# Optimization experiments

Hardware: AMD Instinct MI355X
Metric: run time of the kernel (lower is better)

The kernel has to match this reference:

```python
import jax, jax.numpy as jnp
import numpy as np

EPS = 1e-5
HD = 16          # hidden_dim
OC = 256         # out_chs
NH = 8           # num_heads (groups of qkv conv)
DV = OC // (2 * HD)  # per-head value dim = 8


def conv_bn_silu(x, w, gamma, beta, mean, var, stride=1, pad=1, groups=1):
    # Conv2d(bias=False) + BatchNorm2d(eval) + SiLU, NCHW/OIHW
    y = jax.lax.conv_general_dilated(
        x, w, (stride, stride), [(pad, pad), (pad, pad)],
        dimension_numbers=('NCHW', 'OIHW', 'NCHW'),
        feature_group_count=groups)
    inv = gamma * jax.lax.rsqrt(var + EPS)
    y = y * inv[None, :, None, None] + (beta - mean * inv)[None, :, None, None]
    return y * jax.nn.sigmoid(y)


def _bn_params(key, c):
    k1, k2, k3, k4 = jax.random.split(key, 4)
    g = 1.0 + 0.1 * jax.random.normal(k1, (c,), jnp.float32)
    b = 0.1 * jax.random.normal(k2, (c,), jnp.float32)
    m = 0.1 * jax.random.normal(k3, (c,), jnp.float32)
    v = jax.random.uniform(k4, (c,), jnp.float32, 0.5, 1.5)
    return g, b, m, v


def setup_inputs() -> dict:
    key = jax.random.key(0)
    ks = jax.random.split(key, 8)
    B, C, H, W = 16, 256, 80, 80
    qkv_out = HD * 2 + OC // 2  # 160
    d = {}
    d['x'] = jax.random.normal(ks[0], (B, C, H, W), jnp.float32)
    # qkv_conv: grouped 3x3, groups=NH -> in per group = C//NH
    d['qkv_w'] = jax.random.normal(ks[1], (qkv_out, C // NH, 3, 3), jnp.float32) * 0.05
    d['qkv_g'], d['qkv_b'], d['qkv_m'], d['qkv_v'] = _bn_params(ks[2], qkv_out)
    # hidden_conv: dense 3x3
    d['hid_w'] = jax.random.normal(ks[3], (OC, C, 3, 3), jnp.float32) * 0.02
    d['hid_g'], d['hid_b'], d['hid_m'], d['hid_v'] = _bn_params(ks[4], OC)
    # out_conv: 1x1 on (OC//2*3) channels
    d['out_w'] = jax.random.normal(ks[5], (OC, OC // 2 * 3, 1, 1), jnp.float32) * 0.05
    d['out_g'], d['out_b'], d['out_m'], d['out_v'] = _bn_params(ks[6], OC)
    return d


def reference(x, qkv_w, qkv_g, qkv_b, qkv_m, qkv_v,
              hid_w, hid_g, hid_b, hid_m, hid_v,
              out_w, out_g, out_b, out_m, out_v):
    B, C, H, W = x.shape
    N = H * W
    qkv = conv_bn_silu(x, qkv_w, qkv_g, qkv_b, qkv_m, qkv_v, stride=1, pad=1, groups=NH)
    q = qkv[:, :HD]               # (B, HD, H, W)
    k = qkv[:, HD:2 * HD]
    v = qkv[:, 2 * HD:]           # (B, OC//2, H, W)
    # permute to (B, N, HD) / (B, N, HD, DV), channel-major reshape matches torch .view
    q = q.transpose(0, 2, 3, 1).reshape(B, N, HD)
    k = k.transpose(0, 2, 3, 1).reshape(B, N, HD)
    v = v.transpose(0, 2, 3, 1).reshape(B, N, HD, DV)
    # per-pixel tiny attention: attn[b,n,i,j] = softmax_j(q_i * k_j)
    attn = jax.nn.softmax(q[..., :, None] * k[..., None, :], axis=-1)  # (B,N,HD,HD)
    y = jnp.einsum('bnij,bnjd->bnid', attn, v)                          # (B,N,HD,DV)
    # torch: permute(0,2,3,1).view(B, OC//2, H, W)
    y = y.transpose(0, 2, 3, 1).reshape(B, OC // 2, H, W)
    h = conv_bn_silu(x, hid_w, hid_g, hid_b, hid_m, hid_v, stride=1, pad=1)
    y = jnp.concatenate([y, h], axis=1)  # (B, OC//2*3, H, W)
    return conv_bn_silu(y, out_w, out_g, out_b, out_m, out_v, stride=1, pad=0)
```

## Files before the change

### kernel.cpp

```cpp
#include <hip/hip_runtime.h>
#include <stdint.h>

typedef unsigned short u16;
typedef unsigned int u32;
typedef __attribute__((ext_vector_type(4))) float f32x4;
typedef __attribute__((ext_vector_type(8))) __bf16 bf16x8;

#define EPS_BN 1e-5f

__device__ __forceinline__ u16 f2bf(float f) {
  u32 u = __builtin_bit_cast(u32, f);
  u32 r = (u + 0x7fffu + ((u >> 16) & 1u)) >> 16;
  return (u16)r;
}

__device__ __forceinline__ float silu_f(float v) {
  return v / (1.0f + __expf(-v));
}

__device__ __forceinline__ void gll16(const void* g, void* l) {
  __builtin_amdgcn_global_load_lds(
      (__attribute__((address_space(1))) void*)(void*)g,
      (__attribute__((address_space(3))) void*)l, 16, 0, 0);
}

__global__ __launch_bounds__(256) void prep(
    const float* __restrict__ qkv_w, const float* __restrict__ qg,
    const float* __restrict__ qb, const float* __restrict__ qm,
    const float* __restrict__ qv,
    const float* __restrict__ hid_w, const float* __restrict__ hg,
    const float* __restrict__ hb, const float* __restrict__ hm,
    const float* __restrict__ hv,
    const float* __restrict__ out_w, const float* __restrict__ og,
    const float* __restrict__ ob, const float* __restrict__ om,
    const float* __restrict__ ov,
    u16* __restrict__ wtb, u16* __restrict__ w2b, u16* __restrict__ wqp,
    float* __restrict__ bnq_s, float* __restrict__ bnq_b,
    float* __restrict__ bnh_s, float* __restrict__ bnh_b,
    float* __restrict__ bn2s, float* __restrict__ bn2b,
    float* __restrict__ zpg)
{
  const int gid = blockIdx.x * 256 + threadIdx.x;
  if (gid < 256 * 2304) {
    int j = gid / 2304, k = gid - j * 2304;
    int tap = k >> 8, c = k & 255;
    wtb[gid] = f2bf(hid_w[(j * 256 + c) * 9 + tap]);
  }
  if (gid < 73728) {
    int g = gid / 9216;
    int r = gid - g * 9216;
    int j = r / 288, k = r - j * 288;
    int tap = k >> 5, cg = k & 31;
    float v = 0.f;
    if (j < 20) v = qkv_w[((g * 20 + j) * 32 + cg) * 9 + tap];
    wqp[gid] = f2bf(v);
  }
  if (gid < 98304) w2b[gid] = f2bf(out_w[gid]);
  if (gid < 160) {
    float iv = qg[gid] * rsqrtf(qv[gid] + EPS_BN);
    bnq_s[gid] = iv; bnq_b[gid] = qb[gid] - qm[gid] * iv;
  }
  if (gid < 256) {
    float iv = hg[gid] * rsqrtf(hv[gid] + EPS_BN);
    bnh_s[gid] = iv; bnh_b[gid] = hb[gid] - hm[gid] * iv;
    float iv2 = og[gid] * rsqrtf(ov[gid] + EPS_BN);
    bn2s[gid] = iv2; bn2b[gid] = ob[gid] - om[gid] * iv2;
  }
  if (gid < 64) zpg[gid] = 0.f;
}

__global__ __launch_bounds__(256) void nchw2nhwc(
    const float* __restrict__ x, u16* __restrict__ xn)
{
  __shared__ u16 T[80 * 66];
  const int t = threadIdx.x;
  const int ct = blockIdx.x;
  const int h  = blockIdx.y;
  const int b  = blockIdx.z;
  const float* src = x + ((size_t)b * 256 + ct * 64) * 6400 + h * 80;
  for (int it = 0; it < 5; ++it) {
    int idx = it * 256 + t;
    int cl = idx / 20, w4 = idx - cl * 20;
    float4 v = *(const float4*)(src + (size_t)cl * 6400 + w4 * 4);
    T[(w4 * 4 + 0) * 66 + cl] = f2bf(v.x);
    T[(w4 * 4 + 1) * 66 + cl] = f2bf(v.y);
    T[(w4 * 4 + 2) * 66 + cl] = f2bf(v.z);
    T[(w4 * 4 + 3) * 66 + cl] = f2bf(v.w);
  }
  __syncthreads();
  u16* dst = xn + ((size_t)(b * 80 + h) * 80) * 256 + ct * 64;
  for (int it = 0; it < 5; ++it) {
    int idx = it * 256 + t;
    int wl = idx >> 4;
    int cl = (idx & 15) * 4;
    ushort4 v4;
    v4.x = T[wl * 66 + cl + 0];
    v4.y = T[wl * 66 + cl + 1];
    v4.z = T[wl * 66 + cl + 2];
    v4.w = T[wl * 66 + cl + 3];
    *(ushort4*)(dst + (size_t)wl * 256 + cl) = v4;
  }
}

__global__ __launch_bounds__(256, 2) void gemm_main(
    const u16* __restrict__ xn, const u16* __restrict__ wt,
    const float* __restrict__ bns, const float* __restrict__ bnb,
    const float* __restrict__ zpg, u16* __restrict__ ycat)
{
  __shared__ __attribute__((aligned(16))) u16 Al[128 * 64];
  __shared__ __attribute__((aligned(16))) u16 Bl[128 * 64];
  const int t = threadIdx.x;
  const int wave = t >> 6, lane = t & 63;
  const int wr = wave >> 1, wc = wave & 1;
  const int orig = blockIdx.y * 2 + blockIdx.x;
  const int wg = (orig & 7) * 200 + (orig >> 3);
  const int jtile = (wg / 800) * 128;
  const int ptile = (wg % 800) * 128;

  const int srcc = (((lane & 7) ^ ((lane >> 3) & 7)) * 8);
  int pb[4], hh[4], wwv[4], bofB[4];
#pragma unroll
  for (int c = 0; c < 4; ++c) {
    int m = wave * 32 + c * 8 + (lane >> 3);
    int p = ptile + m;
    pb[c] = p;
    int hw = p % 6400;
    hh[c] = hw / 80;
    wwv[c] = hw - (hw / 80) * 80;
    bofB[c] = (jtile + m) * 2304 + srcc;
  }
  u16* AlW = Al + wave * 2048;
  u16* BlW = Bl + wave * 2048;

  f32x4 acc[4][4];
#pragma unroll
  for (int m = 0; m < 4; ++m)
#pragma unroll
    for (int n = 0; n < 4; ++n) {
      f32x4 z = {0.f, 0.f, 0.f, 0.f};
      acc[m][n] = z;
    }

  for (int ks = 0; ks < 36; ++ks) {
    const int k0 = ks * 64;
    const int tap = k0 >> 8;
    const int c0 = k0 & 255;
    const int dh = tap / 3 - 1, dw = tap - (tap / 3) * 3 - 1;
    __syncthreads();
#pragma unroll
    for (int c = 0; c < 4; ++c) {
      int h2 = hh[c] + dh, w2 = wwv[c] + dw;
      bool ok = ((unsigned)h2 < 80u) & ((unsigned)w2 < 80u);
      const u16* src = ok
          ? (xn + ((size_t)(pb[c] + dh * 80 + dw) * 256 + c0 + srcc))
          : (const u16*)zpg;
      gll16(src, AlW + c * 512);
    }
#pragma unroll
    for (int c = 0; c < 4; ++c)
      gll16(wt + (size_t)(bofB[c] + k0), BlW + c * 512);
    __syncthreads();
#pragma unroll
    for (int kk = 0; kk < 2; ++kk) {
      const int q = kk * 4 + (lane >> 4);
      const int c16 = lane & 15;
      bf16x8 av[4], bv[4];
#pragma unroll
      for (int m = 0; m < 4; ++m) {
        int r = wr * 64 + m * 16 + c16;
        av[m] = *(const bf16x8*)(Al + r * 64 + (q ^ (r & 7)) * 8);
      }
#pragma unroll
      for (int n = 0; n < 4; ++n) {
        int r = wc * 64 + n * 16 + c16;
        bv[n] = *(const bf16x8*)(Bl + r * 64 + (q ^ (r & 7)) * 8);
      }
#pragma unroll
      for (int m = 0; m < 4; ++m)
#pragma unroll
        for (int n = 0; n < 4; ++n)
          acc[m][n] = __builtin_amdgcn_mfma_f32_16x16x32_bf16(
              av[m], bv[n], acc[m][n], 0, 0, 0);
    }
  }

  const int c16 = lane & 15, rg = lane >> 4;
#pragma unroll
  for (int n = 0; n < 4; ++n) {
    int j = jtile + wc * 64 + n * 16 + c16;
    float sc = bns[j], bi = bnb[j];
#pragma unroll
    for (int m = 0; m < 4; ++m) {
      int p0 = ptile + wr * 64 + m * 16 + rg * 4;
#pragma unroll
      for (int r = 0; r < 4; ++r) {
        float v = silu_f(acc[m][n][r] * sc + bi);
        ycat[(size_t)(p0 + r) * 384 + 128 + j] = f2bf(v);
      }
    }
  }
}

__global__ __launch_bounds__(256, 2) void qkv_attn(
    const u16* __restrict__ xn, const u16* __restrict__ wqp,
    const float* __restrict__ bnq_s, const float* __restrict__ bnq_b,
    const float* __restrict__ zpg, u16* __restrict__ ycat)
{
  __shared__ __attribute__((aligned(16))) char LB[81920];
  u16* Al0 = (u16*)LB;
  u16* Al1 = (u16*)(LB + 16384);
  float* qs = (float*)LB;

  const int t = threadIdx.x;
  const int wave = t >> 6, lane = t & 63;
  const int orig = blockIdx.x;
  const int wg = (orig & 7) * 100 + (orig >> 3);
  const int ptile = wg * 128;

  const int srcc = (((lane & 7) ^ ((lane >> 3) & 7)) * 8);
  int pb[4], hh[4], wwv[4];
#pragma unroll
  for (int c = 0; c < 4; ++c) {
    int m = wave * 32 + c * 8 + (lane >> 3);
    int p = ptile + m;
    pb[c] = p;
    int hw = p % 6400;
    hh[c] = hw / 80;
    wwv[c] = hw - (hw / 80) * 80;
  }
  u16* AlW0 = Al0 + wave * 2048;
  u16* AlW1 = Al1 + wave * 2048;

  const int q = lane >> 4, c16 = lane & 15;

  auto STAGE = [&](int tap, int cc, u16* dst) {
    if (tap > 8) tap = 8;
    const int dh = tap / 3 - 1, dw = tap - (tap / 3) * 3 - 1;
    const int dp = dh * 80 + dw;
    const int c0 = cc * 64;
#pragma unroll
    for (int c = 0; c < 4; ++c) {
      int h2 = hh[c] + dh, w2 = wwv[c] + dw;
      bool ok = ((unsigned)h2 < 80u) & ((unsigned)w2 < 80u);
      const u16* src = ok
          ? (xn + ((size_t)(pb[c] + dp) * 256 + c0 + srcc))
          : (const u16*)zpg;
      gll16(src, dst + c * 512);
    }
  };
  auto BQ = [&](int tap, int cc, bf16x8* bv) {
    if (tap > 8) tap = 8;
#pragma unroll
    for (int h = 0; h < 2; ++h)
#pragma unroll
      for (int nf = 0; nf < 2; ++nf) {
        int row = (2 * cc + h) * 32 + nf * 16 + c16;
        bv[h * 2 + nf] =
            *(const bf16x8*)(wqp + (size_t)row * 288 + tap * 32 + q * 8);
      }
  };

  f32x4 acc[2][16];
#pragma unroll
  for (int m = 0; m < 2; ++m)
#pragma unroll
    for (int f = 0; f < 16; ++f) {
      f32x4 z = {0.f, 0.f, 0.f, 0.f};
      acc[m][f] = z;
    }

  bf16x8 bqA[4], bqB[4];
  BQ(0, 0, bqA);
  STAGE(0, 0, AlW0);

  for (int tap = 0; tap < 9; ++tap) {
#pragma unroll
    for (int cc = 0; cc < 4; ++cc) {
      const int ntap = (cc == 3) ? tap + 1 : tap;
      const int ncc = (cc + 1) & 3;
      if ((cc & 1) == 0) { BQ(ntap, ncc, bqB); STAGE(ntap, ncc, AlW1); }
      else               { BQ(ntap, ncc, bqA); STAGE(ntap, ncc, AlW0); }
      asm volatile("s_waitcnt vmcnt(8)" ::: "memory");
      __builtin_amdgcn_sched_barrier(0);
      const u16* AW = ((cc & 1) == 0) ? AlW0 : AlW1;
      const bf16x8* bq = ((cc & 1) == 0) ? bqA : bqB;
      bf16x8 av[2][2];
#pragma unroll
      for (int m = 0; m < 2; ++m) {
        int rl = m * 16 + c16;
#pragma unroll
        for (int h = 0; h < 2; ++h) {
          int q8 = h * 4 + q;
          av[m][h] = *(const bf16x8*)(AW + rl * 64 + ((q8 ^ (rl & 7)) * 8));
        }
      }
#pragma unroll
      for (int h = 0; h < 2; ++h)
#pragma unroll
        for (int m = 0; m < 2; ++m)
#pragma unroll
          for (int nf = 0; nf < 2; ++nf)
            acc[m][(2 * cc + h) * 2 + nf] = __builtin_amdgcn_mfma_f32_16x16x32_bf16(
                av[m][h], bq[h * 2 + nf], acc[m][(2 * cc + h) * 2 + nf], 0, 0, 0);
    }
  }

  asm volatile("s_waitcnt vmcnt(0)" ::: "memory");
  __builtin_amdgcn_sched_barrier(0);
  __syncthreads();

#pragma unroll
  for (int f = 0; f < 16; ++f) {
    int jj = (f & 1) * 16 + c16;
    if (jj >= 20) continue;
    int oc = (f >> 1) * 20 + jj;
    float sc = bnq_s[oc], bi = bnq_b[oc];
#pragma unroll
    for (int m = 0; m < 2; ++m) {
      int pl0 = wave * 32 + m * 16 + q * 4;
#pragma unroll
      for (int r = 0; r < 4; ++r)
        qs[(pl0 + r) * 160 + oc] = silu_f(acc[m][f][r] * sc + bi);
    }
  }
  __syncthreads();

  for (int it = 0; it < 8; ++it) {
    int idx = it * 256 + t;
    int px = idx >> 4, i = idx & 15;
    const float* row = qs + px * 160;
    const float qi = row[i];
    float s[16];
    float mx = -3.4e38f;
#pragma unroll
    for (int j = 0; j < 16; ++j) { s[j] = qi * row[16 + j]; mx = fmaxf(mx, s[j]); }
    float sum = 0.f;
#pragma unroll
    for (int j = 0; j < 16; ++j) { s[j] = __expf(s[j] - mx); sum += s[j]; }
    const float inv = 1.0f / sum;
    float y[8];
#pragma unroll
    for (int d = 0; d < 8; ++d) y[d] = 0.f;
#pragma unroll
    for (int j = 0; j < 16; ++j) {
      const float a = s[j];
      const float* vr = row + 32 + j * 8;
#pragma unroll
      for (int d = 0; d < 8; ++d) y[d] += a * vr[d];
    }
    union { u16 u[8]; uint4 v4; } pk;
#pragma unroll
    for (int d = 0; d < 8; ++d) pk.u[d] = f2bf(y[d] * inv);
    *(uint4*)(ycat + (size_t)(ptile + px) * 384 + i * 8) = pk.v4;
  }
}

__global__ __launch_bounds__(256, 2) void gemm_out(
    const u16* __restrict__ w2, const u16* __restrict__ ycat,
    const float* __restrict__ bns, const float* __restrict__ bnb,
    float* __restrict__ out)
{
  __shared__ __attribute__((aligned(16))) u16 Al[128 * 64];
  __shared__ __attribute__((aligned(16))) u16 Bl[128 * 64];
  const int t = threadIdx.x;
  const int wave = t >> 6, lane = t & 63;
  const int wr = wave >> 1, wc = wave & 1;
  const int orig = blockIdx.y * 2 + blockIdx.x;
  const int wg = (orig & 7) * 200 + (orig >> 3);
  const int octile = (wg / 800) * 128;
  const int ptile = (wg % 800) * 128;

  const int srcc = (((lane & 7) ^ ((lane >> 3) & 7)) * 8);
  int bofA[4], bofB[4];
#pragma unroll
  for (int c = 0; c < 4; ++c) {
    int m = wave * 32 + c * 8 + (lane >> 3);
    bofA[c] = (octile + m) * 384 + srcc;
    bofB[c] = (ptile + m) * 384 + srcc;
  }
  u16* AlW = Al + wave * 2048;
  u16* BlW = Bl + wave * 2048;

  f32x4 acc[4][4];
#pragma unroll
  for (int m = 0; m < 4; ++m)
#pragma unroll
    for (int n = 0; n < 4; ++n) {
      f32x4 z = {0.f, 0.f, 0.f, 0.f};
      acc[m][n] = z;
    }

  for (int ks = 0; ks < 6; ++ks) {
    const int k0 = ks * 64;
    __syncthreads();
#pragma unroll
    for (int c = 0; c < 4; ++c) gll16(w2 + (size_t)(bofA[c] + k0), AlW + c * 512);
#pragma unroll
    for (int c = 0; c < 4; ++c) gll16(ycat + (size_t)(bofB[c] + k0), BlW + c * 512);
    __syncthreads();
#pragma unroll
    for (int kk = 0; kk < 2; ++kk) {
      const int q = kk * 4 + (lane >> 4);
      const int c16 = lane & 15;
      bf16x8 av[4], bv[4];
#pragma unroll
      for (int m = 0; m < 4; ++m) {
        int r = wr * 64 + m * 16 + c16;
        av[m] = *(const bf16x8*)(Al + r * 64 + (q ^ (r & 7)) * 8);
      }
#pragma unroll
      for (int n = 0; n < 4; ++n) {
        int r = wc * 64 + n * 16 + c16;
        bv[n] = *(const bf16x8*)(Bl + r * 64 + (q ^ (r & 7)) * 8);
      }
#pragma unroll
      for (int m = 0; m < 4; ++m)
#pragma unroll
        for (int n = 0; n < 4; ++n)
          acc[m][n] = __builtin_amdgcn_mfma_f32_16x16x32_bf16(
              av[m], bv[n], acc[m][n], 0, 0, 0);
    }
  }

  const int c16 = lane & 15, rg = lane >> 4;
  const int b = ptile / 6400;
  const int hwb = ptile - b * 6400;
#pragma unroll
  for (int m = 0; m < 4; ++m) {
    int oc0 = octile + wr * 64 + m * 16 + rg * 4;
#pragma unroll
    for (int n = 0; n < 4; ++n) {
      int hw = hwb + wc * 64 + n * 16 + c16;
#pragma unroll
      for (int r = 0; r < 4; ++r) {
        int oc = oc0 + r;
        float v = silu_f(acc[m][n][r] * bns[oc] + bnb[oc]);
        out[((size_t)b * 256 + oc) * 6400 + hw] = v;
      }
    }
  }
}

extern "C" void kernel_launch(void* const* d_in, const int* in_sizes, int n_in,
                              void* d_out, int out_size, void* d_ws, size_t ws_size,
                              hipStream_t stream) {
  (void)in_sizes; (void)n_in; (void)out_size; (void)ws_size;
  const float* x    = (const float*)d_in[0];
  const float* qkvw = (const float*)d_in[1];
  const float* qg   = (const float*)d_in[2];
  const float* qb   = (const float*)d_in[3];
  const float* qm   = (const float*)d_in[4];
  const float* qv   = (const float*)d_in[5];
  const float* hw_  = (const float*)d_in[6];
  const float* hg   = (const float*)d_in[7];
  const float* hb   = (const float*)d_in[8];
  const float* hm   = (const float*)d_in[9];
  const float* hv   = (const float*)d_in[10];
  const float* ow   = (const float*)d_in[11];
  const float* og   = (const float*)d_in[12];
  const float* ob   = (const float*)d_in[13];
  const float* om   = (const float*)d_in[14];
  const float* ov   = (const float*)d_in[15];

  char* ws = (char*)d_ws;
  float* zpg   = (float*)(ws + 0);
  float* bnq_s = (float*)(ws + 256);
  float* bnq_b = (float*)(ws + 1280);
  float* bnh_s = (float*)(ws + 2304);
  float* bnh_b = (float*)(ws + 3328);
  float* bn2s  = (float*)(ws + 4352);
  float* bn2b  = (float*)(ws + 5376);
  u16*   wtb   = (u16*)(ws + 6400);
  u16*   w2b   = (u16*)(ws + 1186048);
  u16*   wqp   = (u16*)(ws + 1382656);
  u16*   xn    = (u16*)(ws + 1536000);
  u16*   ycat  = (u16*)(ws + 119500800);
  float* out   = (float*)d_out;

  prep<<<dim3(2304), dim3(256), 0, stream>>>(
      qkvw, qg, qb, qm, qv, hw_, hg, hb, hm, hv, ow, og, ob, om, ov,
      wtb, w2b, wqp, bnq_s, bnq_b, bnh_s, bnh_b, bn2s, bn2b, zpg);
  nchw2nhwc<<<dim3(4, 80, 16), dim3(256), 0, stream>>>(x, xn);
  gemm_main<<<dim3(2, 800), dim3(256), 0, stream>>>(
      xn, wtb, bnh_s, bnh_b, zpg, ycat);
  qkv_attn<<<dim3(800), dim3(256), 0, stream>>>(
      xn, wqp, bnq_s, bnq_b, zpg, ycat);
  gemm_out<<<dim3(2, 800), dim3(256), 0, stream>>>(
      w2b, ycat, bn2s, bn2b, out);
}
```

Baseline: 332.9 us.

## Stage halo tile once per channel chunk and reuse across all nine taps

The qkv grouped conv kernel used to gather a fresh 128-pixel shifted tile from global memory for every tap and channel chunk. It now loads a 320-row halo window of pixels for each 64-channel chunk into LDS once, then reads all nine tap-shifted tiles from that window, masking out-of-image positions to zero in registers. The goal is to cut redundant global and L2 traffic by about nine times. In exchange it uses a larger LDS footprint with double-buffered halos, block-wide barriers between chunks, and weight loads that are no longer prefetched ahead of use.

```diff
diff --git a/kernel.cpp b/kernel.cpp
--- a/kernel.cpp
+++ b/kernel.cpp
@@ -204,11 +204,11 @@
 __global__ __launch_bounds__(256, 2) void qkv_attn(
     const u16* __restrict__ xn, const u16* __restrict__ wqp,
     const float* __restrict__ bnq_s, const float* __restrict__ bnq_b,
-    const float* __restrict__ zpg, u16* __restrict__ ycat)
+    u16* __restrict__ ycat)
 {
   __shared__ __attribute__((aligned(16))) char LB[81920];
-  u16* Al0 = (u16*)LB;
-  u16* Al1 = (u16*)(LB + 16384);
+  u16* HB0 = (u16*)LB;
+  u16* HB1 = (u16*)(LB + 40960);
   float* qs = (float*)LB;
 
   const int t = threadIdx.x;
@@ -216,49 +216,34 @@
   const int orig = blockIdx.x;
   const int wg = (orig & 7) * 100 + (orig >> 3);
   const int ptile = wg * 128;
+  const int pbase = ptile - 88;
 
   const int srcc = (((lane & 7) ^ ((lane >> 3) & 7)) * 8);
-  int pb[4], hh[4], wwv[4];
-#pragma unroll
-  for (int c = 0; c < 4; ++c) {
-    int m = wave * 32 + c * 8 + (lane >> 3);
-    int p = ptile + m;
-    pb[c] = p;
+  const int q = lane >> 4, c16 = lane & 15;
+
+  int ph[2], pw[2];
+#pragma unroll
+  for (int m = 0; m < 2; ++m) {
+    int p = ptile + wave * 32 + m * 16 + c16;
     int hw = p % 6400;
-    hh[c] = hw / 80;
-    wwv[c] = hw - (hw / 80) * 80;
-  }
-  u16* AlW0 = Al0 + wave * 2048;
-  u16* AlW1 = Al1 + wave * 2048;
-
-  const int q = lane >> 4, c16 = lane & 15;
-
-  auto STAGE = [&](int tap, int cc, u16* dst) {
-    if (tap > 8) tap = 8;
-    const int dh = tap / 3 - 1, dw = tap - (tap / 3) * 3 - 1;
-    const int dp = dh * 80 + dw;
-    const int c0 = cc * 64;
-#pragma unroll
-    for (int c = 0; c < 4; ++c) {
-      int h2 = hh[c] + dh, w2 = wwv[c] + dw;
-      bool ok = ((unsigned)h2 < 80u) & ((unsigned)w2 < 80u);
-      const u16* src = ok
-          ? (xn + ((size_t)(pb[c] + dp) * 256 + c0 + srcc))
-          : (const u16*)zpg;
-      gll16(src, dst + c * 512);
+    ph[m] = hw / 80;
+    pw[m] = hw - (hw / 80) * 80;
+  }
+
+  auto STAGE_H = [&](int cc, u16* dst) {
+#pragma unroll
+    for (int r = 0; r < 10; ++r) {
+      int row = r * 32 + wave * 8 + (lane >> 3);
+      int p = pbase + row;
+      int pc = p < 0 ? 0 : (p > 102399 ? 102399 : p);
+      gll16(xn + (size_t)pc * 256 + cc * 64 + srcc,
+            dst + (r * 32 + wave * 8) * 64);
     }
   };
-  auto BQ = [&](int tap, int cc, bf16x8* bv) {
-    if (tap > 8) tap = 8;
-#pragma unroll
-    for (int h = 0; h < 2; ++h)
-#pragma unroll
-      for (int nf = 0; nf < 2; ++nf) {
-        int row = (2 * cc + h) * 32 + nf * 16 + c16;
-        bv[h * 2 + nf] =
-            *(const bf16x8*)(wqp + (size_t)row * 288 + tap * 32 + q * 8);
-      }
-  };
+
+  bf16x8 zv;
+#pragma unroll
+  for (int i = 0; i < 8; ++i) zv[i] = (__bf16)0.0f;
 
   f32x4 acc[2][16];
 #pragma unroll
@@ -269,29 +254,39 @@
       acc[m][f] = z;
     }
 
-  bf16x8 bqA[4], bqB[4];
-  BQ(0, 0, bqA);
-  STAGE(0, 0, AlW0);
-
-  for (int tap = 0; tap < 9; ++tap) {
-#pragma unroll
-    for (int cc = 0; cc < 4; ++cc) {
-      const int ntap = (cc == 3) ? tap + 1 : tap;
-      const int ncc = (cc + 1) & 3;
-      if ((cc & 1) == 0) { BQ(ntap, ncc, bqB); STAGE(ntap, ncc, AlW1); }
-      else               { BQ(ntap, ncc, bqA); STAGE(ntap, ncc, AlW0); }
-      asm volatile("s_waitcnt vmcnt(8)" ::: "memory");
-      __builtin_amdgcn_sched_barrier(0);
-      const u16* AW = ((cc & 1) == 0) ? AlW0 : AlW1;
-      const bf16x8* bq = ((cc & 1) == 0) ? bqA : bqB;
+  STAGE_H(0, HB0);
+  asm volatile("s_waitcnt vmcnt(0)" ::: "memory");
+  __builtin_amdgcn_sched_barrier(0);
+  __syncthreads();
+
+#pragma unroll
+  for (int cc = 0; cc < 4; ++cc) {
+    const u16* HBc = (cc & 1) ? HB1 : HB0;
+    u16* HBn = (cc & 1) ? HB0 : HB1;
+    if (cc < 3) STAGE_H(cc + 1, HBn);
+    for (int tap = 0; tap < 9; ++tap) {
+      const int dh = tap / 3 - 1, dw = tap - (tap / 3) * 3 - 1;
+      const int dp = dh * 80 + dw;
+      bf16x8 bq[2][2];
+#pragma unroll
+      for (int h = 0; h < 2; ++h)
+#pragma unroll
+        for (int nf = 0; nf < 2; ++nf) {
+          int row = (2 * cc + h) * 32 + nf * 16 + c16;
+          bq[h][nf] =
+              *(const bf16x8*)(wqp + (size_t)row * 288 + tap * 32 + q * 8);
+        }
       bf16x8 av[2][2];
 #pragma unroll
       for (int m = 0; m < 2; ++m) {
-        int rl = m * 16 + c16;
+        int rl = wave * 32 + m * 16 + c16 + 88 + dp;
+        bool ok = ((unsigned)(ph[m] + dh) < 80u) &
+                  ((unsigned)(pw[m] + dw) < 80u);
 #pragma unroll
         for (int h = 0; h < 2; ++h) {
           int q8 = h * 4 + q;
-          av[m][h] = *(const bf16x8*)(AW + rl * 64 + ((q8 ^ (rl & 7)) * 8));
+          bf16x8 raw = *(const bf16x8*)(HBc + rl * 64 + ((q8 ^ (rl & 7)) * 8));
+          av[m][h] = ok ? raw : zv;
         }
       }
 #pragma unroll
@@ -301,7 +296,12 @@
 #pragma unroll
           for (int nf = 0; nf < 2; ++nf)
             acc[m][(2 * cc + h) * 2 + nf] = __builtin_amdgcn_mfma_f32_16x16x32_bf16(
-                av[m][h], bq[h * 2 + nf], acc[m][(2 * cc + h) * 2 + nf], 0, 0, 0);
+                av[m][h], bq[h][nf], acc[m][(2 * cc + h) * 2 + nf], 0, 0, 0);
+    }
+    if (cc < 3) {
+      asm volatile("s_waitcnt vmcnt(0)" ::: "memory");
+      __builtin_amdgcn_sched_barrier(0);
+      __syncthreads();
     }
   }
 
@@ -484,7 +484,7 @@
   gemm_main<<<dim3(2, 800), dim3(256), 0, stream>>>(
       xn, wtb, bnh_s, bnh_b, zpg, ycat);
   qkv_attn<<<dim3(800), dim3(256), 0, stream>>>(
-      xn, wqp, bnq_s, bnq_b, zpg, ycat);
+      xn, wqp, bnq_s, bnq_b, ycat);
   gemm_out<<<dim3(2, 800), dim3(256), 0, stream>>>(
       w2b, ycat, bn2s, bn2b, out);
 }
```

Result: faster. 314.5 us (-5.5%).
